# Kernel tuning notes

Measured on AMD Instinct MI355X. Metric: run time of the kernel, lower is better.

Reference implementation:

```python
import jax, jax.numpy as jnp
from jax import lax
import numpy as np

B, C, H, W = 8, 32, 512, 256
HEAD = 64
NUM_PEAKS, RADIUS, THRESH = 18, 5, 0.1
BN_EPS = 1e-5


def setup_inputs() -> dict:
    key = jax.random.key(0)
    ks = jax.random.split(key, 8)
    f32 = jnp.float32
    return {
        "x": jax.random.normal(ks[0], (B, C, H, W), f32),
        # fc_hm head params
        "w1_hm": jax.random.normal(ks[1], (HEAD, C, 3, 3), f32) * 0.05,
        "b1_hm": jnp.zeros((HEAD,), f32),
        "g_hm": jnp.ones((HEAD,), f32),
        "be_hm": jnp.zeros((HEAD,), f32),
        "m_hm": jnp.zeros((HEAD,), f32),
        "v_hm": jnp.ones((HEAD,), f32),
        "w2_hm": jax.random.normal(ks[2], (2, HEAD, 1, 1), f32) * 0.05,
        "b2_hm": jnp.zeros((2,), f32),
        # fc_vec head params
        "w1_vec": jax.random.normal(ks[3], (HEAD, C, 3, 3), f32) * 0.05,
        "b1_vec": jnp.zeros((HEAD,), f32),
        "g_vec": jnp.ones((HEAD,), f32),
        "be_vec": jnp.zeros((HEAD,), f32),
        "m_vec": jnp.zeros((HEAD,), f32),
        "v_vec": jnp.ones((HEAD,), f32),
        "w2_vec": jax.random.normal(ks[4], (2, HEAD, 1, 1), f32) * 0.05,
        "b2_vec": jnp.zeros((2,), f32),
    }


def _conv(x, w, b):
    y = lax.conv_general_dilated(x, w, (1, 1), 'SAME',
                                 dimension_numbers=('NCHW', 'OIHW', 'NCHW'))
    return y + b[None, :, None, None]


def _head(x, w1, b1, g, be, m, v, w2, b2):
    # conv3x3 -> BN(eval) -> ReLU -> (dropout=identity) -> conv final_kernel
    h = _conv(x, w1, b1)
    h = g[None, :, None, None] * (h - m[None, :, None, None]) \
        * lax.rsqrt(v + BN_EPS)[None, :, None, None] + be[None, :, None, None]
    h = jax.nn.relu(h)
    return _conv(h, w2, b2)


def _extract_peaks(hm):
    # hm: [H, W] -> peaks [NUM_PEAKS, 2] as (x, y); iterative argmax + square suppression
    ys = jnp.arange(H)[:, None]
    xs = jnp.arange(W)[None, :]

    def step(hmw, _):
        flat = hmw.reshape(-1)
        idx = jnp.argmax(flat)
        mval = flat[idx]
        y = idx // W
        x = idx % W
        valid = mval > THRESH
        peak = jnp.where(valid,
                         jnp.stack([x, y]).astype(hmw.dtype),
                         jnp.zeros((2,), hmw.dtype))
        sup = (jnp.abs(ys - y) <= RADIUS) & (jnp.abs(xs - x) <= RADIUS)
        hmw = jnp.where(valid & sup, jnp.zeros((), hmw.dtype), hmw)
        return hmw, peak

    _, peaks = lax.scan(step, hm, None, length=NUM_PEAKS)
    return peaks


def _order_points(points):
    # points: [N, 2]; pack valid points sorted by y descending, zeros at the end
    valid = points.sum(axis=1) != 0
    key_y = jnp.where(valid, points[:, 1], -jnp.inf)
    order = jnp.argsort(-key_y)
    p = points[order]
    return jnp.where(valid[order][:, None], p, jnp.zeros((), p.dtype))


def reference(x, w1_hm, b1_hm, g_hm, be_hm, m_hm, v_hm, w2_hm, b2_hm,
              w1_vec, b1_vec, g_vec, be_vec, m_vec, v_vec, w2_vec, b2_vec):
    dual_hm = jax.nn.sigmoid(_head(x, w1_hm, b1_hm, g_hm, be_hm, m_hm, v_hm, w2_hm, b2_hm))  # [B,2,H,W]
    vec_ind = _head(x, w1_vec, b1_vec, g_vec, be_vec, m_vec, v_vec, w2_vec, b2_vec)          # [B,2,H,W]

    peaks = jax.vmap(_extract_peaks)(dual_hm.reshape(B * 2, H, W)).reshape(B, 2, NUM_PEAKS, 2)
    upper = jax.vmap(_order_points)(peaks[:, 0])  # [B,18,2]
    lower = jax.vmap(_order_points)(peaks[:, 1])  # [B,18,2]
    mid = (upper + lower) / 2
    return dual_hm, upper, lower, mid, vec_ind
```

## Files before the change

kernel.cpp:

```cpp
#include <hip/hip_runtime.h>

typedef _Float16 f16;
typedef _Float16 f16x8 __attribute__((ext_vector_type(8)));
typedef float f32x4 __attribute__((ext_vector_type(4)));

#define Bn 8
#define Him 512
#define Wim 256
#define NPK 18
#define RAD 5
#define PTHRESH 0.1f
#define BN_EPS 1e-5f

#define SZ_HM   (Bn*2*Him*Wim)
#define OFF_UP  (SZ_HM)
#define OFF_LO  (OFF_UP + Bn*NPK*2)
#define OFF_MID (OFF_LO + Bn*NPK*2)
#define OFF_VEC (OFF_MID + Bn*NPK*2)

#define PH (Him + 2)
#define PW (Wim + 2)
#define XH_ELT ((size_t)Bn * PH * PW * 32)
#define XH_BYTES (XH_ELT * 2)
#define WBYTES 73728
#define WS_NEED (XH_BYTES + WBYTES + 1024)

#define WS_WBYTES 73728
#define XCOLS 258
#define XSTR  40


__global__ __launch_bounds__(256) void xform_kernel(
    const float* __restrict__ x, f16* __restrict__ xh)
{
    int e = blockIdx.x * 256 + threadIdx.x;
    if (e >= Bn * PH * PW * 4) return;
    int cb  = e & 3;
    int pxl = e >> 2;
    int b   = pxl / (PH * PW);
    int rem = pxl - b * (PH * PW);
    int yy  = rem / PW;
    int xx  = rem - yy * PW;
    int yv = yy - 1, xv = xx - 1;
    f16x8 hv;
    if ((unsigned)yv < (unsigned)Him && (unsigned)xv < (unsigned)Wim) {
        const float* sp = x + (((size_t)b * 32 + cb * 8) * Him + yv) * Wim + xv;
#pragma unroll
        for (int j = 0; j < 8; ++j) hv[j] = (f16)sp[(size_t)j * Him * Wim];
    } else {
#pragma unroll
        for (int j = 0; j < 8; ++j) hv[j] = (f16)0.f;
    }
    *(f16x8*)&xh[(size_t)pxl * 32 + cb * 8] = hv;
}

__global__ __launch_bounds__(256) void prep3_kernel(
    const float* __restrict__ w1_hm, const float* __restrict__ b1_hm,
    const float* __restrict__ g_hm,  const float* __restrict__ be_hm,
    const float* __restrict__ m_hm,  const float* __restrict__ v_hm,
    const float* __restrict__ w1_vec, const float* __restrict__ b1_vec,
    const float* __restrict__ g_vec,  const float* __restrict__ be_vec,
    const float* __restrict__ m_vec,  const float* __restrict__ v_vec,
    void* __restrict__ wreg)
{
    f16* wf = (f16*)wreg;
    float* alpha = (float*)((char*)wreg + WBYTES);
    float* beta  = alpha + 128;

    int e = blockIdx.x * 256 + threadIdx.x;
    int rs = e >> 12;
    int rem = e & 4095;
    int n = rem >> 5;
    int c = rem & 31;
    float v;
    if (n < 64) v = w1_hm[(n * 32 + c) * 9 + rs];
    else        v = w1_vec[((n - 64) * 32 + c) * 9 + rs];
    int byte = rs * 8192 + n * 64 + c * 2;
    byte ^= (n & 7) << 4;
    wf[byte >> 1] = (f16)v;

    if (e < 128) {
        int nn = e;
        float g, be, m, vv, b1;
        if (nn < 64) { g = g_hm[nn]; be = be_hm[nn]; m = m_hm[nn]; vv = v_hm[nn]; b1 = b1_hm[nn]; }
        else { int j = nn - 64; g = g_vec[j]; be = be_vec[j]; m = m_vec[j]; vv = v_vec[j]; b1 = b1_vec[j]; }
        float a = g * rsqrtf(vv + BN_EPS);
        alpha[nn] = a;
        beta[nn]  = a * (b1 - m) + be;
    }
}

__global__ __launch_bounds__(512, 2) void conv5_kernel(
    const f16* __restrict__ xh, const f16* __restrict__ wsw,
    const float* __restrict__ alpha, const float* __restrict__ beta,
    const float* __restrict__ w2_hm, const float* __restrict__ b2_hm,
    const float* __restrict__ w2_vec, const float* __restrict__ b2_vec,
    float* __restrict__ out)
{
    __shared__ __align__(16) f16 s_w[9 * 128 * 32];
    __shared__ __align__(16) f16 s_in[10 * 130 * 32];

    const int hw = blockIdx.x;
    const int logical = (hw & 7) * 128 + (hw >> 3);
    const int b    = logical >> 7;
    const int idx  = logical & 127;
    const int strip = idx >> 1;
    const int half  = idx & 1;
    const int y0  = strip * 8;
    const int x0h = half * 128;

    const int tid  = threadIdx.x;
    const int lane = tid & 63;
    const int wv   = tid >> 6;

    {
        const float4* src = (const float4*)wsw;
        float4* dst = (float4*)s_w;
#pragma unroll
        for (int i = 0; i < 9; ++i) dst[tid + 512 * i] = src[tid + 512 * i];
    }
    {
        const char* xb = (const char*)(xh + (size_t)b * PH * (PW * 32));
        char* sb = (char*)s_in;
        for (int i = tid; i < 5200; i += 512) {
            int row = i / 520;
            int r2  = i - row * 520;
            int px  = r2 >> 2;
            int bo  = (r2 & 3) << 4;
            f16x8 v = *(const f16x8*)(xb + (((size_t)(y0 + row) * PW + (x0h + px)) << 6) + bo);
            int la = ((row * 130 + px) << 6) + bo;
            la ^= (px & 7) << 4;
            *(f16x8*)(sb + la) = v;
        }
    }
    __syncthreads();

    const int l15 = lane & 15;
    const int khB = (lane >> 4) << 4;
    const int sxz = ((l15 << 6) + khB) ^ ((l15 & 7) << 4);
    const char* swb = (const char*)s_w;
    const char* sib = (const char*)s_in;

    float* outhm  = out + ((size_t)b * 2) * Him * Wim + (y0 + wv) * Wim + x0h;
    float* outvec = out + OFF_VEC + ((size_t)b * 2) * Him * Wim + (y0 + wv) * Wim + x0h;

#pragma unroll 1
    for (int xseg = 0; xseg < 2; ++xseg) {
        const int px0s = xseg << 6;

        f32x4 acc[4][8];
#pragma unroll
        for (int pt = 0; pt < 4; ++pt)
#pragma unroll
            for (int nt = 0; nt < 8; ++nt) acc[pt][nt] = (f32x4){0.f, 0.f, 0.f, 0.f};

#pragma unroll 1
        for (int rr = 0; rr < 3; ++rr) {
#pragma unroll 1
            for (int ss = 0; ss < 3; ++ss) {
                f16x8 af[4];
#pragma unroll
                for (int pt = 0; pt < 4; ++pt) {
                    int pxl = px0s + pt * 16 + l15 + ss;
                    int la = (((wv + rr) * 130 + pxl) << 6) + khB;
                    la ^= (pxl & 7) << 4;
                    af[pt] = *(const f16x8*)(sib + la);
                }
                const char* wtap = swb + (rr * 3 + ss) * 8192 + sxz;
#pragma unroll
                for (int nt = 0; nt < 8; ++nt) {
                    f16x8 bf = *(const f16x8*)(wtap + nt * 1024);
                    acc[0][nt] = __builtin_amdgcn_mfma_f32_16x16x32_f16(af[0], bf, acc[0][nt], 0, 0, 0);
                    acc[1][nt] = __builtin_amdgcn_mfma_f32_16x16x32_f16(af[1], bf, acc[1][nt], 0, 0, 0);
                    acc[2][nt] = __builtin_amdgcn_mfma_f32_16x16x32_f16(af[2], bf, acc[2][nt], 0, 0, 0);
                    acc[3][nt] = __builtin_amdgcn_mfma_f32_16x16x32_f16(af[3], bf, acc[3][nt], 0, 0, 0);
                }
            }
        }

        float al[8], bt[8], wa[8], wb[8];
#pragma unroll
        for (int nt = 0; nt < 8; ++nt) {
            int ch = nt * 16 + l15;
            al[nt] = alpha[ch];
            bt[nt] = beta[ch];
            int c6 = ch & 63;
            const float* w2 = (ch < 64) ? w2_hm : w2_vec;
            wa[nt] = w2[c6];
            wb[nt] = w2[64 + c6];
        }
        const float bh0 = b2_hm[0], bh1 = b2_hm[1], bv0 = b2_vec[0], bv1 = b2_vec[1];

#pragma unroll
        for (int pt = 0; pt < 4; ++pt) {
#pragma unroll
            for (int q = 0; q < 4; ++q) {
                float s0 = 0.f, s1 = 0.f, s2 = 0.f, s3 = 0.f;
#pragma unroll
                for (int nt = 0; nt < 8; ++nt) {
                    float h = fmaf(al[nt], acc[pt][nt][q], bt[nt]);
                    h = fmaxf(h, 0.f);
                    if (nt < 4) { s0 = fmaf(wa[nt], h, s0); s1 = fmaf(wb[nt], h, s1); }
                    else        { s2 = fmaf(wa[nt], h, s2); s3 = fmaf(wb[nt], h, s3); }
                }
#pragma unroll
                for (int off = 1; off < 16; off <<= 1) {
                    s0 += __shfl_xor(s0, off);
                    s1 += __shfl_xor(s1, off);
                    s2 += __shfl_xor(s2, off);
                    s3 += __shfl_xor(s3, off);
                }
                int px = px0s + pt * 16 + ((lane >> 4) << 2) + q;
                if (l15 == 0) {
                    outhm[px] = 1.f / (1.f + expf(-(s0 + bh0)));
                } else if (l15 == 1) {
                    outhm[Him * Wim + px] = 1.f / (1.f + expf(-(s1 + bh1)));
                } else if (l15 == 2) {
                    outvec[px] = s2 + bv0;
                } else if (l15 == 3) {
                    outvec[Him * Wim + px] = s3 + bv1;
                }
            }
        }
    }
}


__global__ __launch_bounds__(256) void prep_fb_kernel(
    const float* __restrict__ w1_hm, const float* __restrict__ b1_hm,
    const float* __restrict__ g_hm,  const float* __restrict__ be_hm,
    const float* __restrict__ m_hm,  const float* __restrict__ v_hm,
    const float* __restrict__ w1_vec, const float* __restrict__ b1_vec,
    const float* __restrict__ g_vec,  const float* __restrict__ be_vec,
    const float* __restrict__ m_vec,  const float* __restrict__ v_vec,
    void* __restrict__ wsv)
{
    f16* wf = (f16*)wsv;
    float* alpha = (float*)((char*)wsv + WS_WBYTES);
    float* beta  = alpha + 128;
    int e = blockIdx.x * 256 + threadIdx.x;
    int rs = e >> 12;
    int rem = e & 4095;
    int n = rem >> 5;
    int c = rem & 31;
    float v;
    if (n < 64) v = w1_hm[(n * 32 + c) * 9 + rs];
    else        v = w1_vec[((n - 64) * 32 + c) * 9 + rs];
    wf[e] = (f16)v;
    if (e < 128) {
        int nn = e;
        float g, be, m, vv, b1;
        if (nn < 64) { g = g_hm[nn]; be = be_hm[nn]; m = m_hm[nn]; vv = v_hm[nn]; b1 = b1_hm[nn]; }
        else { int j = nn - 64; g = g_vec[j]; be = be_vec[j]; m = m_vec[j]; vv = v_vec[j]; b1 = b1_vec[j]; }
        float a = g * rsqrtf(vv + BN_EPS);
        alpha[nn] = a;
        beta[nn]  = a * (b1 - m) + be;
    }
}

__global__ __launch_bounds__(256, 1) void conv_fb_kernel(
    const float* __restrict__ x, const void* __restrict__ wsv,
    const float* __restrict__ w2_hm, const float* __restrict__ b2_hm,
    const float* __restrict__ w2_vec, const float* __restrict__ b2_vec,
    float* __restrict__ out)
{
    __shared__ __align__(16) f16 s_x[3 * XCOLS * XSTR];
    __shared__ __align__(16) f16 s_w[9 * 128 * 32];

    const int bid = blockIdx.x;
    const int y = bid & 511;
    const int b = bid >> 9;
    const int tid = threadIdx.x;
    const int lane = tid & 63;
    const int wv = tid >> 6;

    {
        const float4* src = (const float4*)wsv;
        float4* dst = (float4*)s_w;
#pragma unroll
        for (int i = 0; i < 18; ++i) dst[tid + 256 * i] = src[tid + 256 * i];
    }
    {
        const float* xb = x + (size_t)b * 32 * Him * Wim;
#pragma unroll 1
        for (int g = 0; g < 12; ++g) {
            int r  = g >> 2;
            int cb = (g & 3) << 3;
            int gy = y + r - 1;
            bool rowok = (gy >= 0) && (gy < Him);
            {
                int col = tid;
                int gx = col - 1;
                bool ok = rowok && (gx >= 0);
                f16x8 hv;
#pragma unroll
                for (int j = 0; j < 8; ++j) {
                    float v = ok ? xb[(size_t)(cb + j) * (Him * Wim) + gy * Wim + gx] : 0.f;
                    hv[j] = (f16)v;
                }
                *(f16x8*)&s_x[(r * XCOLS + col) * XSTR + cb] = hv;
            }
            if (tid < 2) {
                int col = 256 + tid;
                int gx = col - 1;
                bool ok = rowok && (gx < Wim);
                f16x8 hv;
#pragma unroll
                for (int j = 0; j < 8; ++j) {
                    float v = ok ? xb[(size_t)(cb + j) * (Him * Wim) + gy * Wim + gx] : 0.f;
                    hv[j] = (f16)v;
                }
                *(f16x8*)&s_x[(r * XCOLS + col) * XSTR + cb] = hv;
            }
        }
    }
    __syncthreads();

    const int px0 = wv * 64;
    const int l15 = lane & 15;
    const int khalf = (lane >> 4) << 3;

    f32x4 acc[4][8];
#pragma unroll
    for (int pt = 0; pt < 4; ++pt)
#pragma unroll
        for (int nt = 0; nt < 8; ++nt) acc[pt][nt] = (f32x4){0.f, 0.f, 0.f, 0.f};

#pragma unroll 1
    for (int rs = 0; rs < 9; ++rs) {
        const int rr = rs / 3, ss = rs % 3;
        f16x8 af[4];
#pragma unroll
        for (int pt = 0; pt < 4; ++pt) {
            int col = px0 + pt * 16 + l15 + ss;
            af[pt] = *(const f16x8*)&s_x[(rr * XCOLS + col) * XSTR + khalf];
        }
#pragma unroll
        for (int nt = 0; nt < 8; ++nt) {
            f16x8 bf = *(const f16x8*)&s_w[rs * 4096 + (nt * 16 + l15) * 32 + khalf];
            acc[0][nt] = __builtin_amdgcn_mfma_f32_16x16x32_f16(af[0], bf, acc[0][nt], 0, 0, 0);
            acc[1][nt] = __builtin_amdgcn_mfma_f32_16x16x32_f16(af[1], bf, acc[1][nt], 0, 0, 0);
            acc[2][nt] = __builtin_amdgcn_mfma_f32_16x16x32_f16(af[2], bf, acc[2][nt], 0, 0, 0);
            acc[3][nt] = __builtin_amdgcn_mfma_f32_16x16x32_f16(af[3], bf, acc[3][nt], 0, 0, 0);
        }
    }

    const float* alpha = (const float*)((const char*)wsv + WS_WBYTES);
    const float* beta  = alpha + 128;
    float al[8], bt[8], wa[8], wb[8];
#pragma unroll
    for (int nt = 0; nt < 8; ++nt) {
        int ch = nt * 16 + l15;
        al[nt] = alpha[ch];
        bt[nt] = beta[ch];
        int c6 = ch & 63;
        const float* w2 = (ch < 64) ? w2_hm : w2_vec;
        wa[nt] = w2[c6];
        wb[nt] = w2[64 + c6];
    }
    const float bh0 = b2_hm[0], bh1 = b2_hm[1], bv0 = b2_vec[0], bv1 = b2_vec[1];

    float* outhm  = out + ((size_t)b * 2) * Him * Wim + y * Wim;
    float* outvec = out + OFF_VEC + ((size_t)b * 2) * Him * Wim + y * Wim;

#pragma unroll
    for (int pt = 0; pt < 4; ++pt) {
#pragma unroll
        for (int q = 0; q < 4; ++q) {
            float s0 = 0.f, s1 = 0.f, s2 = 0.f, s3 = 0.f;
#pragma unroll
            for (int nt = 0; nt < 8; ++nt) {
                float h = fmaf(al[nt], acc[pt][nt][q], bt[nt]);
                h = fmaxf(h, 0.f);
                if (nt < 4) { s0 = fmaf(wa[nt], h, s0); s1 = fmaf(wb[nt], h, s1); }
                else        { s2 = fmaf(wa[nt], h, s2); s3 = fmaf(wb[nt], h, s3); }
            }
#pragma unroll
            for (int off = 1; off < 16; off <<= 1) {
                s0 += __shfl_xor(s0, off);
                s1 += __shfl_xor(s1, off);
                s2 += __shfl_xor(s2, off);
                s3 += __shfl_xor(s3, off);
            }
            int px = px0 + pt * 16 + ((lane >> 4) << 2) + q;
            if (l15 == 0) {
                outhm[px] = 1.f / (1.f + expf(-(s0 + bh0)));
            } else if (l15 == 1) {
                outhm[Him * Wim + px] = 1.f / (1.f + expf(-(s1 + bh1)));
            } else if (l15 == 2) {
                outvec[px] = s2 + bv0;
            } else if (l15 == 3) {
                outvec[Him * Wim + px] = s3 + bv1;
            }
        }
    }
}

__global__ __launch_bounds__(1024) void peak_kernel(float* __restrict__ out)
{
    __shared__ float rowval[512];
    __shared__ int   rowcol[512];
    __shared__ int   sbx[NPK], sby[NPK];
    __shared__ int   s_grow;
    __shared__ int   ppx[NPK], ppy[NPK];

    int m = blockIdx.x;
    const float* hm = out + (size_t)m * (Him * Wim);
    int tid  = threadIdx.x;
    int lane = tid & 63;
    int wv   = tid >> 6;

    if (tid < NPK) { ppx[tid] = 0; ppy[tid] = 0; }

#pragma unroll 4
    for (int row = wv; row < 512; row += 16) {
        float4 v4 = *reinterpret_cast<const float4*>(hm + row * 256 + (lane << 2));
        float bv = v4.x; int bc = lane << 2;
        if (v4.y > bv) { bv = v4.y; bc = (lane << 2) + 1; }
        if (v4.z > bv) { bv = v4.z; bc = (lane << 2) + 2; }
        if (v4.w > bv) { bv = v4.w; bc = (lane << 2) + 3; }
#pragma unroll
        for (int off = 32; off; off >>= 1) {
            float ov = __shfl_xor(bv, off);
            int   oc = __shfl_xor(bc, off);
            if (ov > bv || (ov == bv && oc < bc)) { bv = ov; bc = oc; }
        }
        if (lane == 0) { rowval[row] = bv; rowcol[row] = bc; }
    }
    __syncthreads();

    for (int it = 0; it < NPK; ++it) {
        if (wv == 0) {
            float bv = rowval[lane]; int br = lane;
#pragma unroll
            for (int k = 1; k < 8; ++k) {
                float v = rowval[lane + 64 * k];
                if (v > bv) { bv = v; br = lane + 64 * k; }
            }
#pragma unroll
            for (int off = 32; off; off >>= 1) {
                float ov = __shfl_xor(bv, off);
                int   orr = __shfl_xor(br, off);
                if (ov > bv || (ov == bv && orr < br)) { bv = ov; br = orr; }
            }
            if (lane == 0) {
                if (bv > PTHRESH) {
                    int gc = rowcol[br];
                    ppx[it] = gc; ppy[it] = br;
                    sbx[it] = gc; sby[it] = br;
                    s_grow  = br;
                } else {
                    s_grow = -1;
                }
            }
        }
        __syncthreads();
        int grow = s_grow;
        if (grow < 0) break;

        if (wv < 11) {
            int row = grow - RAD + wv;
            if (row >= 0 && row < 512) {
                int nb = it + 1;
                float4 v4 = *reinterpret_cast<const float4*>(hm + row * 256 + (lane << 2));
                float vals[4] = { v4.x, v4.y, v4.z, v4.w };
                float bv2 = -1.f; int bc2 = 0;
#pragma unroll
                for (int q = 0; q < 4; ++q) {
                    int col = (lane << 2) + q;
                    float val = vals[q];
                    for (int i = 0; i < nb; ++i) {
                        int dy = row - sby[i]; if (dy < 0) dy = -dy;
                        int dx = col - sbx[i]; if (dx < 0) dx = -dx;
                        if (dy <= RAD && dx <= RAD) { val = 0.f; break; }
                    }
                    if (val > bv2) { bv2 = val; bc2 = col; }
                }
#pragma unroll
                for (int off = 32; off; off >>= 1) {
                    float ov = __shfl_xor(bv2, off);
                    int   oc = __shfl_xor(bc2, off);
                    if (ov > bv2 || (ov == bv2 && oc < bc2)) { bv2 = ov; bc2 = oc; }
                }
                if (lane == 0) { rowval[row] = bv2; rowcol[row] = bc2; }
            }
        }
        __syncthreads();
    }
    __syncthreads();

    if (tid == 0) {
        float key[NPK]; int ord[NPK];
        for (int i = 0; i < NPK; ++i) {
            int valid = (ppx[i] + ppy[i]) != 0;
            key[i] = valid ? (float)ppy[i] : -3.4e38f;
            ord[i] = i;
        }
        for (int i = 1; i < NPK; ++i) {
            int oi = ord[i]; float ki = key[oi];
            int j = i - 1;
            while (j >= 0 && key[ord[j]] < ki) { ord[j + 1] = ord[j]; --j; }
            ord[j + 1] = oi;
        }
        int bb = m >> 1, which = m & 1;
        float* dst = out + (which ? OFF_LO : OFF_UP) + bb * (NPK * 2);
        for (int i = 0; i < NPK; ++i) {
            int src = ord[i];
            int valid = (ppx[src] + ppy[src]) != 0;
            dst[i * 2 + 0] = valid ? (float)ppx[src] : 0.f;
            dst[i * 2 + 1] = valid ? (float)ppy[src] : 0.f;
        }
    }
}

__global__ __launch_bounds__(320) void mid_kernel(float* __restrict__ out)
{
    int t = threadIdx.x;
    if (t < Bn * NPK * 2)
        out[OFF_MID + t] = 0.5f * (out[OFF_UP + t] + out[OFF_LO + t]);
}

extern "C" void kernel_launch(void* const* d_in, const int* in_sizes, int n_in,
                              void* d_out, int out_size, void* d_ws, size_t ws_size,
                              hipStream_t stream)
{
    const float* x      = (const float*)d_in[0];
    const float* w1_hm  = (const float*)d_in[1];
    const float* b1_hm  = (const float*)d_in[2];
    const float* g_hm   = (const float*)d_in[3];
    const float* be_hm  = (const float*)d_in[4];
    const float* m_hm   = (const float*)d_in[5];
    const float* v_hm   = (const float*)d_in[6];
    const float* w2_hm  = (const float*)d_in[7];
    const float* b2_hm  = (const float*)d_in[8];
    const float* w1_vec = (const float*)d_in[9];
    const float* b1_vec = (const float*)d_in[10];
    const float* g_vec  = (const float*)d_in[11];
    const float* be_vec = (const float*)d_in[12];
    const float* m_vec  = (const float*)d_in[13];
    const float* v_vec  = (const float*)d_in[14];
    const float* w2_vec = (const float*)d_in[15];
    const float* b2_vec = (const float*)d_in[16];

    float* out = (float*)d_out;

    if (ws_size >= (size_t)WS_NEED) {
        f16*  xh   = (f16*)d_ws;
        char* wreg = (char*)d_ws + XH_BYTES;
        const float* alpha = (const float*)(wreg + WBYTES);
        const float* beta  = alpha + 128;

        xform_kernel<<<(Bn * PH * PW * 4 + 255) / 256, 256, 0, stream>>>(x, xh);
        prep3_kernel<<<144, 256, 0, stream>>>(
            w1_hm, b1_hm, g_hm, be_hm, m_hm, v_hm,
            w1_vec, b1_vec, g_vec, be_vec, m_vec, v_vec, wreg);
        conv5_kernel<<<1024, 512, 0, stream>>>(
            xh, (const f16*)wreg, alpha, beta,
            w2_hm, b2_hm, w2_vec, b2_vec, out);
    } else {
        prep_fb_kernel<<<144, 256, 0, stream>>>(
            w1_hm, b1_hm, g_hm, be_hm, m_hm, v_hm,
            w1_vec, b1_vec, g_vec, be_vec, m_vec, v_vec, d_ws);
        conv_fb_kernel<<<Bn * Him, 256, 0, stream>>>(
            x, d_ws, w2_hm, b2_hm, w2_vec, b2_vec, out);
    }

    peak_kernel<<<Bn * 2, 1024, 0, stream>>>(out);

    mid_kernel<<<1, 320, 0, stream>>>(out);
}
```

Before: 294.1 us.

## Swap MFMA operands so channels land in rows and fold BN scale into weights

The conv kernel now feeds weights as the A operand and pixels as the B operand, so each lane's accumulator holds four channels for one pixel. The 1x1 output projection then reduces with two cross-lane shuffles instead of four per output. The BN scale is folded into the fp16 conv weights at prep time, and the shift and 1x1 weights are stored contiguously so they load as float4. The epilogue also switches to the fast __expf, and each lane group writes one output channel for 16 pixels. Folding the scale into fp16 weights changes rounding slightly.

Result: faster. 260.1 us (-11.6%).

```diff
diff --git a/kernel.cpp b/kernel.cpp
--- a/kernel.cpp
+++ b/kernel.cpp
@@ -23,7 +23,7 @@
 #define XH_ELT ((size_t)Bn * PH * PW * 32)
 #define XH_BYTES (XH_ELT * 2)
 #define WBYTES 73728
-#define WS_NEED (XH_BYTES + WBYTES + 1024)
+#define WS_NEED (XH_BYTES + WBYTES + 4096)
 
 #define WS_WBYTES 73728
 #define XCOLS 258
@@ -54,47 +54,52 @@
     *(f16x8*)&xh[(size_t)pxl * 32 + cb * 8] = hv;
 }
 
-__global__ __launch_bounds__(256) void prep3_kernel(
+__global__ __launch_bounds__(256) void prep4_kernel(
     const float* __restrict__ w1_hm, const float* __restrict__ b1_hm,
     const float* __restrict__ g_hm,  const float* __restrict__ be_hm,
     const float* __restrict__ m_hm,  const float* __restrict__ v_hm,
     const float* __restrict__ w1_vec, const float* __restrict__ b1_vec,
     const float* __restrict__ g_vec,  const float* __restrict__ be_vec,
     const float* __restrict__ m_vec,  const float* __restrict__ v_vec,
+    const float* __restrict__ w2_hm,  const float* __restrict__ w2_vec,
     void* __restrict__ wreg)
 {
     f16* wf = (f16*)wreg;
-    float* alpha = (float*)((char*)wreg + WBYTES);
-    float* beta  = alpha + 128;
+    float* btf = (float*)((char*)wreg + WBYTES);
+    float* waf = btf + 128;
+    float* wbf = btf + 256;
 
     int e = blockIdx.x * 256 + threadIdx.x;
     int rs = e >> 12;
     int rem = e & 4095;
     int n = rem >> 5;
     int c = rem & 31;
-    float v;
-    if (n < 64) v = w1_hm[(n * 32 + c) * 9 + rs];
-    else        v = w1_vec[((n - 64) * 32 + c) * 9 + rs];
+
+    float g, vv, v;
+    if (n < 64) { g = g_hm[n]; vv = v_hm[n]; v = w1_hm[(n * 32 + c) * 9 + rs]; }
+    else { int j = n - 64; g = g_vec[j]; vv = v_vec[j]; v = w1_vec[(j * 32 + c) * 9 + rs]; }
+    float al = g * rsqrtf(vv + BN_EPS);
     int byte = rs * 8192 + n * 64 + c * 2;
     byte ^= (n & 7) << 4;
-    wf[byte >> 1] = (f16)v;
+    wf[byte >> 1] = (f16)(v * al);
 
     if (e < 128) {
         int nn = e;
-        float g, be, m, vv, b1;
-        if (nn < 64) { g = g_hm[nn]; be = be_hm[nn]; m = m_hm[nn]; vv = v_hm[nn]; b1 = b1_hm[nn]; }
-        else { int j = nn - 64; g = g_vec[j]; be = be_vec[j]; m = m_vec[j]; vv = v_vec[j]; b1 = b1_vec[j]; }
-        float a = g * rsqrtf(vv + BN_EPS);
-        alpha[nn] = a;
-        beta[nn]  = a * (b1 - m) + be;
-    }
-}
-
-__global__ __launch_bounds__(512, 2) void conv5_kernel(
+        float gg, be, m, vvv, b1;
+        if (nn < 64) { gg = g_hm[nn]; be = be_hm[nn]; m = m_hm[nn]; vvv = v_hm[nn]; b1 = b1_hm[nn]; }
+        else { int j = nn - 64; gg = g_vec[j]; be = be_vec[j]; m = m_vec[j]; vvv = v_vec[j]; b1 = b1_vec[j]; }
+        float a = gg * rsqrtf(vvv + BN_EPS);
+        btf[nn] = a * (b1 - m) + be;
+        if (nn < 64) { waf[nn] = w2_hm[nn]; wbf[nn] = w2_hm[64 + nn]; }
+        else { int j = nn - 64; waf[nn] = w2_vec[j]; wbf[nn] = w2_vec[64 + j]; }
+    }
+}
+
+__global__ __launch_bounds__(512, 2) void conv7_kernel(
     const f16* __restrict__ xh, const f16* __restrict__ wsw,
-    const float* __restrict__ alpha, const float* __restrict__ beta,
-    const float* __restrict__ w2_hm, const float* __restrict__ b2_hm,
-    const float* __restrict__ w2_vec, const float* __restrict__ b2_vec,
+    const float* __restrict__ btf, const float* __restrict__ waf,
+    const float* __restrict__ wbf,
+    const float* __restrict__ b2_hm, const float* __restrict__ b2_vec,
     float* __restrict__ out)
 {
     __shared__ __align__(16) f16 s_w[9 * 128 * 32];
@@ -136,7 +141,8 @@
     __syncthreads();
 
     const int l15 = lane & 15;
-    const int khB = (lane >> 4) << 4;
+    const int g   = lane >> 4;
+    const int khB = g << 4;
     const int sxz = ((l15 << 6) + khB) ^ ((l15 & 7) << 4);
     const char* swb = (const char*)s_w;
     const char* sib = (const char*)s_in;
@@ -148,11 +154,11 @@
     for (int xseg = 0; xseg < 2; ++xseg) {
         const int px0s = xseg << 6;
 
-        f32x4 acc[4][8];
-#pragma unroll
-        for (int pt = 0; pt < 4; ++pt)
-#pragma unroll
-            for (int nt = 0; nt < 8; ++nt) acc[pt][nt] = (f32x4){0.f, 0.f, 0.f, 0.f};
+        f32x4 acc[8][4];
+#pragma unroll
+        for (int ct = 0; ct < 8; ++ct)
+#pragma unroll
+            for (int nt = 0; nt < 4; ++nt) acc[ct][nt] = (f32x4){0.f, 0.f, 0.f, 0.f};
 
 #pragma unroll 1
         for (int rr = 0; rr < 3; ++rr) {
@@ -160,66 +166,88 @@
             for (int ss = 0; ss < 3; ++ss) {
                 f16x8 af[4];
 #pragma unroll
-                for (int pt = 0; pt < 4; ++pt) {
-                    int pxl = px0s + pt * 16 + l15 + ss;
+                for (int nt = 0; nt < 4; ++nt) {
+                    int pxl = px0s + nt * 16 + l15 + ss;
                     int la = (((wv + rr) * 130 + pxl) << 6) + khB;
                     la ^= (pxl & 7) << 4;
-                    af[pt] = *(const f16x8*)(sib + la);
+                    af[nt] = *(const f16x8*)(sib + la);
                 }
                 const char* wtap = swb + (rr * 3 + ss) * 8192 + sxz;
 #pragma unroll
-                for (int nt = 0; nt < 8; ++nt) {
-                    f16x8 bf = *(const f16x8*)(wtap + nt * 1024);
-                    acc[0][nt] = __builtin_amdgcn_mfma_f32_16x16x32_f16(af[0], bf, acc[0][nt], 0, 0, 0);
-                    acc[1][nt] = __builtin_amdgcn_mfma_f32_16x16x32_f16(af[1], bf, acc[1][nt], 0, 0, 0);
-                    acc[2][nt] = __builtin_amdgcn_mfma_f32_16x16x32_f16(af[2], bf, acc[2][nt], 0, 0, 0);
-                    acc[3][nt] = __builtin_amdgcn_mfma_f32_16x16x32_f16(af[3], bf, acc[3][nt], 0, 0, 0);
-                }
-            }
-        }
-
-        float al[8], bt[8], wa[8], wb[8];
-#pragma unroll
-        for (int nt = 0; nt < 8; ++nt) {
-            int ch = nt * 16 + l15;
-            al[nt] = alpha[ch];
-            bt[nt] = beta[ch];
-            int c6 = ch & 63;
-            const float* w2 = (ch < 64) ? w2_hm : w2_vec;
-            wa[nt] = w2[c6];
-            wb[nt] = w2[64 + c6];
-        }
+                for (int ct = 0; ct < 8; ++ct) {
+                    f16x8 wfr = *(const f16x8*)(wtap + ct * 1024);
+                    acc[ct][0] = __builtin_amdgcn_mfma_f32_16x16x32_f16(wfr, af[0], acc[ct][0], 0, 0, 0);
+                    acc[ct][1] = __builtin_amdgcn_mfma_f32_16x16x32_f16(wfr, af[1], acc[ct][1], 0, 0, 0);
+                    acc[ct][2] = __builtin_amdgcn_mfma_f32_16x16x32_f16(wfr, af[2], acc[ct][2], 0, 0, 0);
+                    acc[ct][3] = __builtin_amdgcn_mfma_f32_16x16x32_f16(wfr, af[3], acc[ct][3], 0, 0, 0);
+                }
+            }
+        }
+
+        float s[4][4];
+#pragma unroll
+        for (int nt = 0; nt < 4; ++nt)
+#pragma unroll
+            for (int o = 0; o < 4; ++o) s[nt][o] = 0.f;
+
+        const int cb0 = g << 2;
+#pragma unroll
+        for (int ct = 0; ct < 8; ++ct) {
+            const float4 bt4 = *(const float4*)&btf[ct * 16 + cb0];
+            const float4 wa4 = *(const float4*)&waf[ct * 16 + cb0];
+            const float4 wb4 = *(const float4*)&wbf[ct * 16 + cb0];
+            float btq[4] = { bt4.x, bt4.y, bt4.z, bt4.w };
+            float waq[4] = { wa4.x, wa4.y, wa4.z, wa4.w };
+            float wbq[4] = { wb4.x, wb4.y, wb4.z, wb4.w };
+#pragma unroll
+            for (int nt = 0; nt < 4; ++nt) {
+#pragma unroll
+                for (int q = 0; q < 4; ++q) {
+                    float h = fmaxf(acc[ct][nt][q] + btq[q], 0.f);
+                    if (ct < 4) {
+                        s[nt][0] = fmaf(waq[q], h, s[nt][0]);
+                        s[nt][1] = fmaf(wbq[q], h, s[nt][1]);
+                    } else {
+                        s[nt][2] = fmaf(waq[q], h, s[nt][2]);
+                        s[nt][3] = fmaf(wbq[q], h, s[nt][3]);
+                    }
+                }
+            }
+        }
+#pragma unroll
+        for (int nt = 0; nt < 4; ++nt)
+#pragma unroll
+            for (int o = 0; o < 4; ++o) {
+                s[nt][o] += __shfl_xor(s[nt][o], 16);
+                s[nt][o] += __shfl_xor(s[nt][o], 32);
+            }
+
         const float bh0 = b2_hm[0], bh1 = b2_hm[1], bv0 = b2_vec[0], bv1 = b2_vec[1];
-
-#pragma unroll
-        for (int pt = 0; pt < 4; ++pt) {
-#pragma unroll
-            for (int q = 0; q < 4; ++q) {
-                float s0 = 0.f, s1 = 0.f, s2 = 0.f, s3 = 0.f;
-#pragma unroll
-                for (int nt = 0; nt < 8; ++nt) {
-                    float h = fmaf(al[nt], acc[pt][nt][q], bt[nt]);
-                    h = fmaxf(h, 0.f);
-                    if (nt < 4) { s0 = fmaf(wa[nt], h, s0); s1 = fmaf(wb[nt], h, s1); }
-                    else        { s2 = fmaf(wa[nt], h, s2); s3 = fmaf(wb[nt], h, s3); }
-                }
-#pragma unroll
-                for (int off = 1; off < 16; off <<= 1) {
-                    s0 += __shfl_xor(s0, off);
-                    s1 += __shfl_xor(s1, off);
-                    s2 += __shfl_xor(s2, off);
-                    s3 += __shfl_xor(s3, off);
-                }
-                int px = px0s + pt * 16 + ((lane >> 4) << 2) + q;
-                if (l15 == 0) {
-                    outhm[px] = 1.f / (1.f + expf(-(s0 + bh0)));
-                } else if (l15 == 1) {
-                    outhm[Him * Wim + px] = 1.f / (1.f + expf(-(s1 + bh1)));
-                } else if (l15 == 2) {
-                    outvec[px] = s2 + bv0;
-                } else if (l15 == 3) {
-                    outvec[Him * Wim + px] = s3 + bv1;
-                }
+        if (g == 0) {
+#pragma unroll
+            for (int nt = 0; nt < 4; ++nt) {
+                int px = px0s + nt * 16 + l15;
+                float e = __expf(-(s[nt][0] + bh0));
+                outhm[px] = 1.f / (1.f + e);
+            }
+        } else if (g == 1) {
+#pragma unroll
+            for (int nt = 0; nt < 4; ++nt) {
+                int px = px0s + nt * 16 + l15;
+                float e = __expf(-(s[nt][1] + bh1));
+                outhm[Him * Wim + px] = 1.f / (1.f + e);
+            }
+        } else if (g == 2) {
+#pragma unroll
+            for (int nt = 0; nt < 4; ++nt) {
+                int px = px0s + nt * 16 + l15;
+                outvec[px] = s[nt][2] + bv0;
+            }
+        } else {
+#pragma unroll
+            for (int nt = 0; nt < 4; ++nt) {
+                int px = px0s + nt * 16 + l15;
+                outvec[Him * Wim + px] = s[nt][3] + bv1;
             }
         }
     }
@@ -547,16 +575,18 @@
     if (ws_size >= (size_t)WS_NEED) {
         f16*  xh   = (f16*)d_ws;
         char* wreg = (char*)d_ws + XH_BYTES;
-        const float* alpha = (const float*)(wreg + WBYTES);
-        const float* beta  = alpha + 128;
+        const float* btf = (const float*)(wreg + WBYTES);
+        const float* waf = btf + 128;
+        const float* wbf = btf + 256;
 
         xform_kernel<<<(Bn * PH * PW * 4 + 255) / 256, 256, 0, stream>>>(x, xh);
-        prep3_kernel<<<144, 256, 0, stream>>>(
+        prep4_kernel<<<144, 256, 0, stream>>>(
             w1_hm, b1_hm, g_hm, be_hm, m_hm, v_hm,
-            w1_vec, b1_vec, g_vec, be_vec, m_vec, v_vec, wreg);
-        conv5_kernel<<<1024, 512, 0, stream>>>(
-            xh, (const f16*)wreg, alpha, beta,
-            w2_hm, b2_hm, w2_vec, b2_vec, out);
+            w1_vec, b1_vec, g_vec, be_vec, m_vec, v_vec,
+            w2_hm, w2_vec, wreg);
+        conv7_kernel<<<1024, 512, 0, stream>>>(
+            xh, (const f16*)wreg, btf, waf, wbf,
+            b2_hm, b2_vec, out);
     } else {
         prep_fb_kernel<<<144, 256, 0, stream>>>(
             w1_hm, b1_hm, g_hm, be_hm, m_hm, v_hm,
```
